# Performance work log

Hardware: AMD Instinct MI355X
Metric: run time of the kernel (lower is better)

Reference implementation:

```python
import jax, jax.numpy as jnp
import numpy as np

B, N, D, H = 4, 2048, 256, 4
HD = D // H


def _linear(x, W, b):
    return x @ W.T + b


def _rotate_half(x):
    # pairs (x0,x1) -> (-x1, x0)
    x1 = x[..., ::2]
    x2 = x[..., 1::2]
    return jnp.stack((-x2, x1), axis=-1).reshape(x.shape)


def _layernorm(x, g, b, eps=1e-5):
    m = jnp.mean(x, axis=-1, keepdims=True)
    v = jnp.mean((x - m) ** 2, axis=-1, keepdims=True)
    return (x - m) / jnp.sqrt(v + eps) * g + b


def _ffn(x, W1, b1, g, be, W2, b2):
    h = _linear(x, W1, b1)
    h = _layernorm(h, g, be)
    h = jax.nn.gelu(h, approximate=False)
    return _linear(h, W2, b2)


def _self_block(x, enc, Wqkv, bqkv, Wout, bout, W1, b1, g, be, W2, b2):
    Bq, Nq, _ = x.shape
    qkv = _linear(x, Wqkv, bqkv).reshape(Bq, Nq, H, HD, 3).transpose(0, 2, 1, 3, 4)  # [B,H,N,HD,3]
    q, k, v = qkv[..., 0], qkv[..., 1], qkv[..., 2]
    q = q * enc[0] + _rotate_half(q) * enc[1]
    k = k * enc[0] + _rotate_half(k) * enc[1]
    scale = HD ** -0.5
    sim = jnp.einsum('bhid,bhjd->bhij', q, k) * scale
    attn = jax.nn.softmax(sim, axis=-1)
    ctx = jnp.einsum('bhij,bhjd->bhid', attn, v)
    msg = _linear(ctx.transpose(0, 2, 1, 3).reshape(Bq, Nq, D), Wout, bout)
    return x + _ffn(jnp.concatenate([x, msg], axis=-1), W1, b1, g, be, W2, b2)


def _cross_block(x0, x1, Wqk, bqk, Wv, bv, Wo, bo, W1, b1, g, be, W2, b2):
    def heads(t):
        return t.reshape(t.shape[0], t.shape[1], H, HD).transpose(0, 2, 1, 3)  # [B,H,N,HD]
    qk0 = heads(_linear(x0, Wqk, bqk))
    qk1 = heads(_linear(x1, Wqk, bqk))
    v0 = heads(_linear(x0, Wv, bv))
    v1 = heads(_linear(x1, Wv, bv))
    s = (HD ** -0.5) ** 0.5
    qk0 = qk0 * s
    qk1 = qk1 * s
    sim = jnp.einsum('bhid,bhjd->bhij', qk0, qk1)
    attn01 = jax.nn.softmax(sim, axis=-1)   # over j (x1 tokens)
    attn10 = jax.nn.softmax(sim, axis=-2)   # over i (x0 tokens)
    m0 = jnp.einsum('bhij,bhjd->bhid', attn01, v1)
    m1 = jnp.einsum('bhij,bhid->bhjd', attn10, v0)
    def unheads(t):
        return t.transpose(0, 2, 1, 3).reshape(t.shape[0], t.shape[2], D)
    m0 = _linear(unheads(m0), Wo, bo)
    m1 = _linear(unheads(m1), Wo, bo)
    x0 = x0 + _ffn(jnp.concatenate([x0, m0], axis=-1), W1, b1, g, be, W2, b2)
    x1 = x1 + _ffn(jnp.concatenate([x1, m1], axis=-1), W1, b1, g, be, W2, b2)
    return x0, x1


def setup_inputs() -> dict:
    key = jax.random.key(0)
    ks = jax.random.split(key, 32)
    std = 0.05

    def rn(k, shape, s=std):
        return jax.random.normal(k, shape, dtype=jnp.float32) * s

    def enc(k):
        ang = jax.random.uniform(k, (B, 1, N, HD // 2), dtype=jnp.float32) * (2 * np.pi)
        cos = jnp.repeat(jnp.cos(ang), 2, axis=-1)
        sin = jnp.repeat(jnp.sin(ang), 2, axis=-1)
        return jnp.stack([cos, sin], axis=0)  # [2,B,1,N,HD]

    return {
        'desc0': rn(ks[0], (B, N, D), 1.0),
        'desc1': rn(ks[1], (B, N, D), 1.0),
        'enc0': enc(ks[2]),
        'enc1': enc(ks[3]),
        's_Wqkv': rn(ks[4], (3 * D, D)), 's_bqkv': jnp.zeros((3 * D,), jnp.float32),
        's_Wout': rn(ks[5], (D, D)), 's_bout': jnp.zeros((D,), jnp.float32),
        's_W1': rn(ks[6], (2 * D, 2 * D)), 's_b1': jnp.zeros((2 * D,), jnp.float32),
        's_g': jnp.ones((2 * D,), jnp.float32), 's_be': jnp.zeros((2 * D,), jnp.float32),
        's_W2': rn(ks[7], (D, 2 * D)), 's_b2': jnp.zeros((D,), jnp.float32),
        'c_Wqk': rn(ks[8], (D, D)), 'c_bqk': jnp.zeros((D,), jnp.float32),
        'c_Wv': rn(ks[9], (D, D)), 'c_bv': jnp.zeros((D,), jnp.float32),
        'c_Wo': rn(ks[10], (D, D)), 'c_bo': jnp.zeros((D,), jnp.float32),
        'c_W1': rn(ks[11], (2 * D, 2 * D)), 'c_b1': jnp.zeros((2 * D,), jnp.float32),
        'c_g': jnp.ones((2 * D,), jnp.float32), 'c_be': jnp.zeros((2 * D,), jnp.float32),
        'c_W2': rn(ks[12], (D, 2 * D)), 'c_b2': jnp.zeros((D,), jnp.float32),
    }


def reference(desc0, desc1, enc0, enc1,
              s_Wqkv, s_bqkv, s_Wout, s_bout, s_W1, s_b1, s_g, s_be, s_W2, s_b2,
              c_Wqk, c_bqk, c_Wv, c_bv, c_Wo, c_bo, c_W1, c_b1, c_g, c_be, c_W2, c_b2):
    d0 = _self_block(desc0, enc0, s_Wqkv, s_bqkv, s_Wout, s_bout, s_W1, s_b1, s_g, s_be, s_W2, s_b2)
    d1 = _self_block(desc1, enc1, s_Wqkv, s_bqkv, s_Wout, s_bout, s_W1, s_b1, s_g, s_be, s_W2, s_b2)
    return _cross_block(d0, d1, c_Wqk, c_bqk, c_Wv, c_bv, c_Wo, c_bo, c_W1, c_b1, c_g, c_be, c_W2, c_b2)
```

## Files before the change

kernel.cpp:

```cpp
#include <hip/hip_runtime.h>
#include <cstddef>

#define NTOK 2048
#define BDIM 4
#define DIM 256
#define NHEAD 4
#define MROWS 8192
#define M2 16384
#define NMu ((size_t)MROWS * DIM)

typedef unsigned short u16;
typedef __attribute__((ext_vector_type(8))) short short8;
typedef __attribute__((ext_vector_type(4))) float f32x4;

#if __has_builtin(__builtin_amdgcn_exp2f)
#define EXP2(x) __builtin_amdgcn_exp2f(x)
#else
#define EXP2(x) exp2f(x)
#endif

__device__ __forceinline__ u16 f2bf(float x) {
  union { float f; unsigned u; } c; c.f = x;
  unsigned r = c.u + 0x7FFFu + ((c.u >> 16) & 1u);
  return (u16)(r >> 16);
}
__device__ __forceinline__ float bf2f(u16 u) {
  union { unsigned u; float f; } c; c.u = ((unsigned)u) << 16;
  return c.f;
}

__device__ __forceinline__ void glds16(const void* g, void* l) {
  __builtin_amdgcn_global_load_lds(
      (const __attribute__((address_space(1))) unsigned int*)g,
      (__attribute__((address_space(3))) unsigned int*)l, 16, 0, 0);
}

__global__ __launch_bounds__(256) void gemm_bf16_kernel(
    const u16* __restrict__ A, int lda,
    const u16* __restrict__ A2, int lda2, int kSplit,
    const u16* __restrict__ W,
    const float* __restrict__ bias0, const float* __restrict__ bias1,
    int nsplit, float os0, float os1,
    u16* __restrict__ Yb0, int ldy0,
    u16* __restrict__ Yb1, int ldy1,
    int K)
{
  __shared__ u16 As[2 * 4096];
  __shared__ u16 Bs[2 * 4096];
  const int t = threadIdx.x;
  const int m0 = blockIdx.y * 128, n0 = blockIdx.x * 128;
  const int r4 = t >> 2, c8 = (t & 3) * 8;
  const int lane = t & 63, w = t >> 6;
  const int cl = lane & 15, quad = lane >> 4;
  const int wm = (w >> 1) * 64, wn = (w & 1) * 64;

  f32x4 acc[4][4];
#pragma unroll
  for (int i = 0; i < 4; ++i)
#pragma unroll
    for (int j = 0; j < 4; ++j) acc[i][j] = (f32x4){0.f, 0.f, 0.f, 0.f};

  for (int k0 = 0; k0 < K; k0 += 64) {
    const u16* Ab; int la; int kk;
    if (k0 < kSplit) { Ab = A; la = lda; kk = k0; }
    else             { Ab = A2; la = lda2; kk = k0 - kSplit; }
    const u16* ag = Ab + (size_t)(m0 + r4) * la + kk + c8;
    const u16* bg = W + (size_t)(n0 + r4) * K + k0 + c8;
    __syncthreads();
#pragma unroll
    for (int kh = 0; kh < 2; ++kh) {
      glds16(ag + kh * 32, &As[kh * 4096 + t * 8]);
      glds16(ag + (size_t)64 * la + kh * 32, &As[kh * 4096 + 2048 + t * 8]);
      glds16(bg + kh * 32, &Bs[kh * 4096 + t * 8]);
      glds16(bg + (size_t)64 * K + kh * 32, &Bs[kh * 4096 + 2048 + t * 8]);
    }
    __syncthreads();

#pragma unroll
    for (int kh = 0; kh < 2; ++kh) {
      short8 af[4], bfr[4];
#pragma unroll
      for (int i = 0; i < 4; ++i)
        af[i] = *(const short8*)&As[kh * 4096 + (wm + i * 16 + cl) * 32 + quad * 8];
#pragma unroll
      for (int i = 0; i < 4; ++i)
        bfr[i] = *(const short8*)&Bs[kh * 4096 + (wn + i * 16 + cl) * 32 + quad * 8];
#pragma unroll
      for (int mt = 0; mt < 4; ++mt)
#pragma unroll
        for (int nt = 0; nt < 4; ++nt)
          acc[mt][nt] = __builtin_amdgcn_mfma_f32_16x16x32_bf16(
              af[mt], bfr[nt], acc[mt][nt], 0, 0, 0);
    }
  }

#pragma unroll
  for (int mt = 0; mt < 4; ++mt)
#pragma unroll
    for (int nt = 0; nt < 4; ++nt) {
      const int colg = n0 + wn + nt * 16 + cl;
      const bool first = colg < nsplit;
      const int c2 = first ? colg : colg - nsplit;
      const float bs = first ? bias0[c2] : bias1[c2];
      const float os = first ? os0 : os1;
      u16* yb = first ? Yb0 : Yb1;
      const int ly = first ? ldy0 : ldy1;
#pragma unroll
      for (int r = 0; r < 4; ++r) {
        const int rowg = m0 + wm + mt * 16 + quad * 4 + r;
        yb[(size_t)rowg * ly + c2] = f2bf((acc[mt][nt][r] + bs) * os);
      }
    }
}

__global__ __launch_bounds__(256) void gemm64_kernel(
    const u16* __restrict__ A, int lda,
    const u16* __restrict__ W,
    const float* __restrict__ bias,
    const u16* __restrict__ resb, int ldrb,
    float* __restrict__ Yf, int ldyf,
    u16* __restrict__ Yb, int ldyb,
    int K)
{
  __shared__ u16 As[2 * 2048];
  __shared__ u16 Bs[2 * 2048];
  const int t = threadIdx.x;
  const int m0 = blockIdx.y * 64, n0 = blockIdx.x * 64;
  const int r8 = t >> 2, c8 = (t & 3) * 8;
  const int lane = t & 63, w = t >> 6;
  const int cl = lane & 15, quad = lane >> 4;
  const int wm = (w >> 1) * 32, wn = (w & 1) * 32;

  f32x4 acc[2][2];
#pragma unroll
  for (int i = 0; i < 2; ++i)
#pragma unroll
    for (int j = 0; j < 2; ++j) acc[i][j] = (f32x4){0.f, 0.f, 0.f, 0.f};

  for (int k0 = 0; k0 < K; k0 += 64) {
    const u16* ag = A + (size_t)(m0 + r8) * lda + k0 + c8;
    const u16* bg = W + (size_t)(n0 + r8) * K + k0 + c8;
    __syncthreads();
#pragma unroll
    for (int kh = 0; kh < 2; ++kh) {
      glds16(ag + kh * 32, &As[kh * 2048 + t * 8]);
      glds16(bg + kh * 32, &Bs[kh * 2048 + t * 8]);
    }
    __syncthreads();

#pragma unroll
    for (int kh = 0; kh < 2; ++kh) {
      short8 af[2], bfr[2];
#pragma unroll
      for (int i = 0; i < 2; ++i)
        af[i] = *(const short8*)&As[kh * 2048 + (wm + i * 16 + cl) * 32 + quad * 8];
#pragma unroll
      for (int j = 0; j < 2; ++j)
        bfr[j] = *(const short8*)&Bs[kh * 2048 + (wn + j * 16 + cl) * 32 + quad * 8];
#pragma unroll
      for (int mt = 0; mt < 2; ++mt)
#pragma unroll
        for (int nt = 0; nt < 2; ++nt)
          acc[mt][nt] = __builtin_amdgcn_mfma_f32_16x16x32_bf16(
              af[mt], bfr[nt], acc[mt][nt], 0, 0, 0);
    }
  }

#pragma unroll
  for (int mt = 0; mt < 2; ++mt)
#pragma unroll
    for (int nt = 0; nt < 2; ++nt) {
      const int colg = n0 + wn + nt * 16 + cl;
      const float bs = bias[colg];
#pragma unroll
      for (int r = 0; r < 4; ++r) {
        const int rowg = m0 + wm + mt * 16 + quad * 4 + r;
        float v = acc[mt][nt][r] + bs;
        if (resb) v += bf2f(resb[(size_t)rowg * ldrb + colg]);
        if (Yf) Yf[(size_t)rowg * ldyf + colg] = v;
        if (Yb) Yb[(size_t)rowg * ldyb + colg] = f2bf(v);
      }
    }
}

__global__ __launch_bounds__(256) void wfuse_kernel(
    const float* __restrict__ W1, const float* __restrict__ Wo,
    const float* __restrict__ b1, const float* __restrict__ bo,
    const float* __restrict__ cW1, const float* __restrict__ cWo,
    const float* __restrict__ cb1, const float* __restrict__ cbo,
    u16* __restrict__ W1f, u16* __restrict__ cW1f,
    float* __restrict__ b1f, float* __restrict__ cb1f)
{
  const int n = blockIdx.x, sel = blockIdx.y;
  const float* Ws = sel ? cW1 : W1;
  const float* Wos = sel ? cWo : Wo;
  u16* out = sel ? cW1f : W1f;
  __shared__ float rowh[256];
  const int t = threadIdx.x;
  rowh[t] = Ws[(size_t)n * 512 + 256 + t];
  out[(size_t)n * 512 + t] = f2bf(Ws[(size_t)n * 512 + t]);
  __syncthreads();
  float acc = 0.f;
  for (int m = 0; m < 256; ++m) acc += rowh[m] * Wos[(size_t)m * 256 + t];
  out[(size_t)n * 512 + 256 + t] = f2bf(acc);
  if (t == 0) {
    const float* bos = sel ? cbo : bo;
    const float* b1s = sel ? cb1 : b1;
    float a = b1s[n];
    for (int m = 0; m < 256; ++m) a += rowh[m] * bos[m];
    (sel ? cb1f : b1f)[n] = a;
  }
}

__global__ __launch_bounds__(256) void rope_repack_kernel(
    const u16* __restrict__ qkv, const float* __restrict__ enc0,
    const float* __restrict__ enc1,
    u16* __restrict__ Q, u16* __restrict__ K, u16* __restrict__ V)
{
  const int idx = blockIdx.x * blockDim.x + threadIdx.x;
  const int i = idx & 31;
  const int h = (idx >> 5) & 3;
  const int m = idx >> 7;
  const int half = m >> 13;
  const int lm = m & (MROWS - 1);
  const float* enc = half ? enc1 : enc0;
  const u16* src = qkv + (size_t)m * 768 + h * 192 + i * 6;
  const unsigned a0 = *(const unsigned*)(src);
  const unsigned a1 = *(const unsigned*)(src + 2);
  const unsigned a2 = *(const unsigned*)(src + 4);
  const float q0 = bf2f((u16)a0), k0 = bf2f((u16)(a0 >> 16));
  const float v0 = bf2f((u16)a1), q1 = bf2f((u16)(a1 >> 16));
  const float k1 = bf2f((u16)a2), v1 = bf2f((u16)(a2 >> 16));
  const float c = enc[(size_t)lm * 64 + 2 * i];
  const float s = enc[(size_t)MROWS * 64 + (size_t)lm * 64 + 2 * i];
  const float QSC = 0.18033688011112042f;
  const size_t o = (size_t)m * 256 + h * 64 + 2 * i;
  *(unsigned*)(Q + o) = (unsigned)f2bf((q0 * c - q1 * s) * QSC) |
                        ((unsigned)f2bf((q1 * c + q0 * s) * QSC) << 16);
  *(unsigned*)(K + o) = (unsigned)f2bf(k0 * c - k1 * s) |
                        ((unsigned)f2bf(k1 * c + k0 * s) << 16);
  *(unsigned*)(V + o) = (unsigned)f2bf(v0) | ((unsigned)f2bf(v1) << 16);
}

__global__ __launch_bounds__(256) void transpose_v_kernel(
    const u16* __restrict__ in, u16* __restrict__ out)
{
  __shared__ u16 Tl[64][72];
  const int bz = blockIdx.z, h = blockIdx.y;
  const int n0 = blockIdx.x * 64;
  const int t = threadIdx.x;
  {
    const int row = t >> 2, c16 = (t & 3) * 16;
    const u16* src = in + (size_t)(bz * NTOK + n0 + row) * 256 + h * 64 + c16;
    *(uint4*)&Tl[row][c16] = *(const uint4*)src;
    *(uint4*)&Tl[row][c16 + 8] = *(const uint4*)(src + 8);
  }
  __syncthreads();
  const int d = t >> 2, qr = t & 3;
  union { u16 u[16]; uint4 v[2]; } pk;
#pragma unroll
  for (int j = 0; j < 16; ++j) pk.u[j] = Tl[qr * 16 + j][d];
  u16* dst = out + ((size_t)((bz * NHEAD + h) * 64 + d)) * NTOK + n0 + qr * 16;
  *(uint4*)dst = pk.v[0];
  *(uint4*)(dst + 8) = pk.v[1];
}

__global__ __launch_bounds__(256, 2) void attn5_kernel(
    const u16* __restrict__ Qb, const u16* __restrict__ Kb,
    const u16* __restrict__ Vtb, u16* __restrict__ Ou, int cross)
{
  __shared__ u16 Ks[2][64 * 64];
  __shared__ u16 Vs[2][64 * 64];
  __shared__ u16 Ps[4][32 * 64];

  const int hw = blockIdx.x;
  const int li = hw >> 3;
  const int y  = (hw & 7) * 4 + (li >> 4);
  const int n0 = (li & 15) * 128;

  const int h2 = y >> 4, b = (y >> 2) & 3, h = y & 3;
  const int kh = cross ? (1 - h2) : h2;
  const int qrowbase = (h2 * 4 + b) * NTOK;
  const int krowbase = (kh * 4 + b) * NTOK;
  const int vz = kh * 4 + b;
  const int t = threadIdx.x, lane = t & 63, w = t >> 6;
  const int cl = lane & 15, quad = lane >> 4;
  const int q0 = w * 32;
  const int fsw = (cl & 7) << 4;

  short8 bq[2][2];
#pragma unroll
  for (int c = 0; c < 2; ++c) {
    const u16* qsrc = Qb + (size_t)(qrowbase + n0 + q0 + c * 16 + cl) * 256 +
                      h * 64 + quad * 8;
    bq[c][0] = *(const short8*)qsrc;
    bq[c][1] = *(const short8*)(qsrc + 32);
  }

  float l_r[2] = {0.f, 0.f};
  f32x4 o[2][4];
#pragma unroll
  for (int c = 0; c < 2; ++c)
#pragma unroll
    for (int i = 0; i < 4; ++i) o[c][i] = (f32x4){0.f, 0.f, 0.f, 0.f};

  const int srow = t >> 2;
  const int scb = (t & 3) * 32;
  const int ssw = (srow & 7) << 4;
  const u16* Kg = Kb + (size_t)(krowbase + srow) * 256 + h * 64 + (t & 3) * 16;
  const u16* Vg = Vtb + ((size_t)(vz * NHEAD + h) * 64 + srow) * NTOK + (t & 3) * 16;

  uint4 ka0 = *(const uint4*)Kg, ka1 = *(const uint4*)(Kg + 8);
  uint4 va0 = *(const uint4*)Vg, va1 = *(const uint4*)(Vg + 8);
  {
    char* kd = (char*)&Ks[0][srow * 64];
    *(uint4*)(kd + (scb ^ ssw)) = ka0;
    *(uint4*)(kd + ((scb + 16) ^ ssw)) = ka1;
    char* vd = (char*)&Vs[0][srow * 64];
    *(uint4*)(vd + (scb ^ ssw)) = va0;
    *(uint4*)(vd + ((scb + 16) ^ ssw)) = va1;
  }
  Kg += 64 * 256; Vg += 64;
  ka0 = *(const uint4*)Kg; ka1 = *(const uint4*)(Kg + 8);
  va0 = *(const uint4*)Vg; va1 = *(const uint4*)(Vg + 8);
  __syncthreads();

  for (int tile = 0; tile < 32; ++tile) {
    const int cur = tile & 1, nxt = cur ^ 1;

    f32x4 sf[2][4];
    __builtin_amdgcn_s_setprio(1);
#pragma unroll
    for (int kb = 0; kb < 4; ++kb) {
      const char* kr = (const char*)&Ks[cur][(kb * 16 + cl) * 64];
      short8 ak0 = *(const short8*)(kr + ((quad * 16) ^ fsw));
      short8 ak1 = *(const short8*)(kr + ((quad * 16 + 64) ^ fsw));
#pragma unroll
      for (int c = 0; c < 2; ++c) {
        f32x4 acc = (f32x4){0.f, 0.f, 0.f, 0.f};
        acc = __builtin_amdgcn_mfma_f32_16x16x32_bf16(ak0, bq[c][0], acc, 0, 0, 0);
        acc = __builtin_amdgcn_mfma_f32_16x16x32_bf16(ak1, bq[c][1], acc, 0, 0, 0);
        sf[c][kb] = acc;
      }
    }
    __builtin_amdgcn_s_setprio(0);

    if (tile < 31) {
      char* kd = (char*)&Ks[nxt][srow * 64];
      *(uint4*)(kd + (scb ^ ssw)) = ka0;
      *(uint4*)(kd + ((scb + 16) ^ ssw)) = ka1;
      if (tile < 30) {
        Kg += 64 * 256;
        ka0 = *(const uint4*)Kg; ka1 = *(const uint4*)(Kg + 8);
      }
    }

#pragma unroll
    for (int c = 0; c < 2; ++c) {
      float rs = 0.f;
#pragma unroll
      for (int kb = 0; kb < 4; ++kb)
#pragma unroll
        for (int r = 0; r < 4; ++r) {
          const float p = EXP2(sf[c][kb][r]);
          sf[c][kb][r] = p; rs += p;
        }
      rs += __shfl_xor(rs, 16);
      rs += __shfl_xor(rs, 32);
      l_r[c] += rs;
      char* pd = (char*)&Ps[w][(c * 16 + cl) * 64];
#pragma unroll
      for (int kb = 0; kb < 4; ++kb) {
        unsigned d0 = __builtin_amdgcn_perm(__float_as_uint(sf[c][kb][1]),
                                            __float_as_uint(sf[c][kb][0]), 0x07060302u);
        unsigned d1 = __builtin_amdgcn_perm(__float_as_uint(sf[c][kb][3]),
                                            __float_as_uint(sf[c][kb][2]), 0x07060302u);
        uint2 pk; pk.x = d0; pk.y = d1;
        *(uint2*)(pd + ((kb * 32 + quad * 8) ^ fsw)) = pk;
      }
    }

    short8 bp[2][2];
#pragma unroll
    for (int c = 0; c < 2; ++c) {
      const char* pr = (const char*)&Ps[w][(c * 16 + cl) * 64];
      bp[c][0] = *(const short8*)(pr + ((quad * 16) ^ fsw));
      bp[c][1] = *(const short8*)(pr + ((quad * 16 + 64) ^ fsw));
    }
    __builtin_amdgcn_s_setprio(1);
#pragma unroll
    for (int db = 0; db < 4; ++db) {
      const char* vr = (const char*)&Vs[cur][(db * 16 + cl) * 64];
      short8 av0 = *(const short8*)(vr + ((quad * 16) ^ fsw));
      short8 av1 = *(const short8*)(vr + ((quad * 16 + 64) ^ fsw));
#pragma unroll
      for (int c = 0; c < 2; ++c) {
        o[c][db] = __builtin_amdgcn_mfma_f32_16x16x32_bf16(av0, bp[c][0], o[c][db], 0, 0, 0);
        o[c][db] = __builtin_amdgcn_mfma_f32_16x16x32_bf16(av1, bp[c][1], o[c][db], 0, 0, 0);
      }
    }
    __builtin_amdgcn_s_setprio(0);

    if (tile < 31) {
      char* vd = (char*)&Vs[nxt][srow * 64];
      *(uint4*)(vd + (scb ^ ssw)) = va0;
      *(uint4*)(vd + ((scb + 16) ^ ssw)) = va1;
      if (tile < 30) {
        Vg += 64;
        va0 = *(const uint4*)Vg; va1 = *(const uint4*)(Vg + 8);
      }
    }
    __syncthreads();
  }

#pragma unroll
  for (int c = 0; c < 2; ++c) {
    const float inv = 1.f / l_r[c];
    const size_t rowo = (size_t)(qrowbase + n0 + q0 + c * 16 + cl) * 256 + h * 64;
#pragma unroll
    for (int db = 0; db < 4; ++db) {
      ushort4 st;
      st.x = f2bf(o[c][db][0] * inv); st.y = f2bf(o[c][db][1] * inv);
      st.z = f2bf(o[c][db][2] * inv); st.w = f2bf(o[c][db][3] * inv);
      *(ushort4*)(Ou + rowo + db * 16 + quad * 4) = st;
    }
  }
}

__global__ __launch_bounds__(256) void ln_gelu_kernel(
    const u16* __restrict__ Hm, const float* __restrict__ g,
    const float* __restrict__ be, u16* __restrict__ out)
{
  const int rowi = blockIdx.x * 4 + (threadIdx.x >> 6);
  const int lane = threadIdx.x & 63;
  const u16* row = Hm + (size_t)rowi * 512 + lane * 8;
  u16* orow = out + (size_t)rowi * 512 + lane * 8;
  uint4 raw = *(const uint4*)row;
  float x[8];
  const unsigned* rw = (const unsigned*)&raw;
#pragma unroll
  for (int i = 0; i < 4; ++i) {
    x[2 * i]     = bf2f((u16)rw[i]);
    x[2 * i + 1] = bf2f((u16)(rw[i] >> 16));
  }
  float s = 0.f;
#pragma unroll
  for (int i = 0; i < 8; ++i) s += x[i];
#pragma unroll
  for (int off = 32; off; off >>= 1) s += __shfl_xor(s, off);
  const float mean = s * (1.f / 512.f);
  float s2 = 0.f;
#pragma unroll
  for (int i = 0; i < 8; ++i) { const float d = x[i] - mean; s2 += d * d; }
#pragma unroll
  for (int off = 32; off; off >>= 1) s2 += __shfl_xor(s2, off);
  const float rstd = rsqrtf(s2 * (1.f / 512.f) + 1e-5f);
  unsigned ov[4];
#pragma unroll
  for (int i = 0; i < 4; ++i) {
    const int c = lane * 8 + 2 * i;
    const float y0 = (x[2 * i] - mean) * rstd * g[c] + be[c];
    const float y1 = (x[2 * i + 1] - mean) * rstd * g[c + 1] + be[c + 1];
    const float g0 = 0.5f * y0 * (1.f + erff(y0 * 0.70710678118654752f));
    const float g1 = 0.5f * y1 * (1.f + erff(y1 * 0.70710678118654752f));
    ov[i] = (unsigned)f2bf(g0) | ((unsigned)f2bf(g1) << 16);
  }
  *(uint4*)orow = *(uint4*)ov;
}

__global__ __launch_bounds__(256) void pack_all_kernel(
    const float* w0, const float* w1, const float* w2, const float* w3,
    const float* w4, const float* d0, const float* d1,
    u16* __restrict__ wb, u16* __restrict__ descb)
{
  const size_t idx4 = ((size_t)blockIdx.x * 256 + threadIdx.x) * 4;
  const float* src; u16* dst; size_t off;
  if (idx4 < 589824) {
    off = idx4; dst = wb + idx4;
    if      (idx4 < 196608) { src = w0; }
    else if (idx4 < 327680) { src = w1; off -= 196608; }
    else if (idx4 < 393216) { src = w2; off -= 327680; }
    else if (idx4 < 458752) { src = w3; off -= 393216; }
    else                    { src = w4; off -= 458752; }
  } else {
    size_t o = idx4 - 589824;
    dst = descb + o;
    if (o < NMu) { src = d0; off = o; }
    else         { src = d1; off = o - NMu; }
  }
  float4 v = *(const float4*)(src + off);
  ushort4 ov;
  ov.x = f2bf(v.x); ov.y = f2bf(v.y); ov.z = f2bf(v.z); ov.w = f2bf(v.w);
  *(ushort4*)dst = ov;
}

extern "C" void kernel_launch(void* const* d_in, const int* in_sizes, int n_in,
                              void* d_out, int out_size, void* d_ws, size_t ws_size,
                              hipStream_t stream) {
  const float* desc0  = (const float*)d_in[0];
  const float* desc1  = (const float*)d_in[1];
  const float* enc0   = (const float*)d_in[2];
  const float* enc1   = (const float*)d_in[3];
  const float* s_Wqkv = (const float*)d_in[4];
  const float* s_bqkv = (const float*)d_in[5];
  const float* s_Wout = (const float*)d_in[6];
  const float* s_bout = (const float*)d_in[7];
  const float* s_W1   = (const float*)d_in[8];
  const float* s_b1   = (const float*)d_in[9];
  const float* s_g    = (const float*)d_in[10];
  const float* s_be   = (const float*)d_in[11];
  const float* s_W2   = (const float*)d_in[12];
  const float* s_b2   = (const float*)d_in[13];
  const float* c_Wqk  = (const float*)d_in[14];
  const float* c_bqk  = (const float*)d_in[15];
  const float* c_Wv   = (const float*)d_in[16];
  const float* c_bv   = (const float*)d_in[17];
  const float* c_Wo   = (const float*)d_in[18];
  const float* c_bo   = (const float*)d_in[19];
  const float* c_W1   = (const float*)d_in[20];
  const float* c_b1   = (const float*)d_in[21];
  const float* c_g    = (const float*)d_in[22];
  const float* c_be   = (const float*)d_in[23];
  const float* c_W2   = (const float*)d_in[24];
  const float* c_b2   = (const float*)d_in[25];

  u16* U = (u16*)d_ws;
  u16* descb = U + 0 * NMu;
  u16* qkvb  = U + 2 * NMu;
  u16* ctxb  = U + 2 * NMu;
  u16* Qu    = U + 8 * NMu;
  u16* Ku    = U + 10 * NMu;
  u16* Vu    = U + 12 * NMu;
  u16* Vt    = U + 14 * NMu;
  u16* hbufb = U + 12 * NMu;
  u16* hb2   = U + 16 * NMu;
  float* b1f = (float*)(U + 20 * NMu);
  float* cb1f = b1f + 512;
  u16* s_b   = U + 21 * NMu;
  u16* wb    = U + 23 * NMu;

  u16* Wqkvb = wb;
  u16* W2b   = wb + 196608;
  u16* cQKVb = wb + 327680;
  u16* cW2b  = wb + 458752;
  u16* W1f   = wb + 589824;
  u16* cW1f  = wb + 851968;

  float* outf = (float*)d_out;

  const dim3 tv_grid(NTOK / 64, NHEAD, 8);
  const int rope_blocks = (M2 * 128) / 256;
  const int lng_blocks  = M2 / 4;
  const float csc = 0.42466090014400953f;

  hipLaunchKernelGGL(pack_all_kernel, dim3(4672), dim3(256), 0, stream,
                     s_Wqkv, s_W2, c_Wqk, c_Wv, c_W2, desc0, desc1, wb, descb);
  hipLaunchKernelGGL(wfuse_kernel, dim3(512, 2), dim3(256), 0, stream,
                     s_W1, s_Wout, s_b1, s_bout, c_W1, c_Wo, c_b1, c_bo,
                     W1f, cW1f, b1f, cb1f);

  hipLaunchKernelGGL(gemm_bf16_kernel, dim3(6, 128), dim3(256), 0, stream,
                     descb, 256, (const u16*)nullptr, 0, 1 << 30, Wqkvb,
                     s_bqkv, (const float*)nullptr, 1 << 30, 1.f, 1.f,
                     qkvb, 768, (u16*)nullptr, 0, 256);
  hipLaunchKernelGGL(rope_repack_kernel, dim3(rope_blocks), dim3(256), 0, stream,
                     qkvb, enc0, enc1, Qu, Ku, Vu);
  hipLaunchKernelGGL(transpose_v_kernel, tv_grid, dim3(256), 0, stream, Vu, Vt);
  hipLaunchKernelGGL(attn5_kernel, dim3(512), dim3(256), 0, stream,
                     Qu, Ku, Vt, ctxb, 0);
  hipLaunchKernelGGL(gemm_bf16_kernel, dim3(4, 128), dim3(256), 0, stream,
                     descb, 256, ctxb, 256, 256, W1f,
                     b1f, (const float*)nullptr, 1 << 30, 1.f, 1.f,
                     hbufb, 512, (u16*)nullptr, 0, 512);
  hipLaunchKernelGGL(ln_gelu_kernel, dim3(lng_blocks), dim3(256), 0, stream,
                     hbufb, s_g, s_be, hb2);
  hipLaunchKernelGGL(gemm64_kernel, dim3(4, 256), dim3(256), 0, stream,
                     hb2, 512, W2b, s_b2, descb, 256,
                     (float*)nullptr, 0, s_b, 256, 512);

  u16* qkb = Qu;
  u16* vb  = Ku;
  hipLaunchKernelGGL(gemm_bf16_kernel, dim3(4, 128), dim3(256), 0, stream,
                     s_b, 256, (const u16*)nullptr, 0, 1 << 30, cQKVb,
                     c_bqk, c_bv, 256, csc, 1.f,
                     qkb, 256, vb, 256, 256);
  hipLaunchKernelGGL(transpose_v_kernel, tv_grid, dim3(256), 0, stream, vb, Vt);
  hipLaunchKernelGGL(attn5_kernel, dim3(512), dim3(256), 0, stream,
                     qkb, qkb, Vt, ctxb, 1);
  hipLaunchKernelGGL(gemm_bf16_kernel, dim3(4, 128), dim3(256), 0, stream,
                     s_b, 256, ctxb, 256, 256, cW1f,
                     cb1f, (const float*)nullptr, 1 << 30, 1.f, 1.f,
                     hbufb, 512, (u16*)nullptr, 0, 512);
  hipLaunchKernelGGL(ln_gelu_kernel, dim3(lng_blocks), dim3(256), 0, stream,
                     hbufb, c_g, c_be, hb2);
  hipLaunchKernelGGL(gemm64_kernel, dim3(4, 256), dim3(256), 0, stream,
                     hb2, 512, cW2b, c_b2, s_b, 256,
                     outf, 256, (u16*)nullptr, 0, 512);
}
```

Baseline: 372.9 us.

## Merge weight pack with weight fusion, and fuse RoPE repack with V transpose

Folds the bf16 packing kernel and the weight-fusion kernel into one launch by splitting on block index. Also fuses the RoPE/QKV repack with the V transpose: V tiles are staged in shared memory and written straight out transposed, so the intermediate V buffer and its extra global round trip go away. The fused RoPE kernel launches only 256 blocks, each looping 32 times, which lowers parallelism compared with the previous 8192-block launch. Two kernel launches are removed.

```diff
diff --git a/kernel.cpp b/kernel.cpp
--- a/kernel.cpp
+++ b/kernel.cpp
@@ -183,7 +183,10 @@
     }
 }
 
-__global__ __launch_bounds__(256) void wfuse_kernel(
+__global__ __launch_bounds__(256) void pack_wfuse_kernel(
+    const float* w0, const float* w1, const float* w2, const float* w3,
+    const float* w4, const float* d0, const float* d1,
+    u16* __restrict__ wb, u16* __restrict__ descb,
     const float* __restrict__ W1, const float* __restrict__ Wo,
     const float* __restrict__ b1, const float* __restrict__ bo,
     const float* __restrict__ cW1, const float* __restrict__ cWo,
@@ -191,55 +194,101 @@
     u16* __restrict__ W1f, u16* __restrict__ cW1f,
     float* __restrict__ b1f, float* __restrict__ cb1f)
 {
-  const int n = blockIdx.x, sel = blockIdx.y;
-  const float* Ws = sel ? cW1 : W1;
-  const float* Wos = sel ? cWo : Wo;
-  u16* out = sel ? cW1f : W1f;
   __shared__ float rowh[256];
+  const int bid = blockIdx.x;
   const int t = threadIdx.x;
-  rowh[t] = Ws[(size_t)n * 512 + 256 + t];
-  out[(size_t)n * 512 + t] = f2bf(Ws[(size_t)n * 512 + t]);
-  __syncthreads();
-  float acc = 0.f;
-  for (int m = 0; m < 256; ++m) acc += rowh[m] * Wos[(size_t)m * 256 + t];
-  out[(size_t)n * 512 + 256 + t] = f2bf(acc);
-  if (t == 0) {
-    const float* bos = sel ? cbo : bo;
-    const float* b1s = sel ? cb1 : b1;
-    float a = b1s[n];
-    for (int m = 0; m < 256; ++m) a += rowh[m] * bos[m];
-    (sel ? cb1f : b1f)[n] = a;
-  }
-}
-
-__global__ __launch_bounds__(256) void rope_repack_kernel(
+  if (bid < 4672) {
+    const size_t idx4 = ((size_t)bid * 256 + t) * 4;
+    const float* src; u16* dst; size_t off;
+    if (idx4 < 589824) {
+      off = idx4; dst = wb + idx4;
+      if      (idx4 < 196608) { src = w0; }
+      else if (idx4 < 327680) { src = w1; off -= 196608; }
+      else if (idx4 < 393216) { src = w2; off -= 327680; }
+      else if (idx4 < 458752) { src = w3; off -= 393216; }
+      else                    { src = w4; off -= 458752; }
+    } else {
+      size_t o = idx4 - 589824;
+      dst = descb + o;
+      if (o < NMu) { src = d0; off = o; }
+      else         { src = d1; off = o - NMu; }
+    }
+    float4 v = *(const float4*)(src + off);
+    ushort4 ov;
+    ov.x = f2bf(v.x); ov.y = f2bf(v.y); ov.z = f2bf(v.z); ov.w = f2bf(v.w);
+    *(ushort4*)dst = ov;
+  } else {
+    const int idx = bid - 4672;
+    const int n = idx & 511, sel = idx >> 9;
+    const float* Ws = sel ? cW1 : W1;
+    const float* Wos = sel ? cWo : Wo;
+    u16* out = sel ? cW1f : W1f;
+    rowh[t] = Ws[(size_t)n * 512 + 256 + t];
+    out[(size_t)n * 512 + t] = f2bf(Ws[(size_t)n * 512 + t]);
+    __syncthreads();
+    float acc = 0.f;
+    for (int m = 0; m < 256; ++m) acc += rowh[m] * Wos[(size_t)m * 256 + t];
+    out[(size_t)n * 512 + 256 + t] = f2bf(acc);
+    if (t == 0) {
+      const float* bos = sel ? cbo : bo;
+      const float* b1s = sel ? cb1 : b1;
+      float a = b1s[n];
+      for (int m = 0; m < 256; ++m) a += rowh[m] * bos[m];
+      (sel ? cb1f : b1f)[n] = a;
+    }
+  }
+}
+
+__global__ __launch_bounds__(256) void rope_tv_kernel(
     const u16* __restrict__ qkv, const float* __restrict__ enc0,
     const float* __restrict__ enc1,
-    u16* __restrict__ Q, u16* __restrict__ K, u16* __restrict__ V)
+    u16* __restrict__ Q, u16* __restrict__ K, u16* __restrict__ Vt)
 {
-  const int idx = blockIdx.x * blockDim.x + threadIdx.x;
-  const int i = idx & 31;
-  const int h = (idx >> 5) & 3;
-  const int m = idx >> 7;
-  const int half = m >> 13;
-  const int lm = m & (MROWS - 1);
-  const float* enc = half ? enc1 : enc0;
-  const u16* src = qkv + (size_t)m * 768 + h * 192 + i * 6;
-  const unsigned a0 = *(const unsigned*)(src);
-  const unsigned a1 = *(const unsigned*)(src + 2);
-  const unsigned a2 = *(const unsigned*)(src + 4);
-  const float q0 = bf2f((u16)a0), k0 = bf2f((u16)(a0 >> 16));
-  const float v0 = bf2f((u16)a1), q1 = bf2f((u16)(a1 >> 16));
-  const float k1 = bf2f((u16)a2), v1 = bf2f((u16)(a2 >> 16));
-  const float c = enc[(size_t)lm * 64 + 2 * i];
-  const float s = enc[(size_t)MROWS * 64 + (size_t)lm * 64 + 2 * i];
+  __shared__ u16 Vl[64 * 264];
+  const int blk = blockIdx.x;
+  const int t = threadIdx.x;
+  const int hf = blk >> 7;
+  const float* enc = hf ? enc1 : enc0;
   const float QSC = 0.18033688011112042f;
-  const size_t o = (size_t)m * 256 + h * 64 + 2 * i;
-  *(unsigned*)(Q + o) = (unsigned)f2bf((q0 * c - q1 * s) * QSC) |
-                        ((unsigned)f2bf((q1 * c + q0 * s) * QSC) << 16);
-  *(unsigned*)(K + o) = (unsigned)f2bf(k0 * c - k1 * s) |
-                        ((unsigned)f2bf(k1 * c + k0 * s) << 16);
-  *(unsigned*)(V + o) = (unsigned)f2bf(v0) | ((unsigned)f2bf(v1) << 16);
+
+  for (int p = 0; p < 32; ++p) {
+    const int j = p * 256 + t;
+    const int i = j & 31;
+    const int h = (j >> 5) & 3;
+    const int lt = j >> 7;
+    const int m = blk * 64 + lt;
+    const int lm = m & (MROWS - 1);
+    const u16* src = qkv + (size_t)m * 768 + h * 192 + i * 6;
+    const unsigned a0 = *(const unsigned*)(src);
+    const unsigned a1 = *(const unsigned*)(src + 2);
+    const unsigned a2 = *(const unsigned*)(src + 4);
+    const float q0 = bf2f((u16)a0), k0 = bf2f((u16)(a0 >> 16));
+    const float v0 = bf2f((u16)a1), q1 = bf2f((u16)(a1 >> 16));
+    const float k1 = bf2f((u16)a2), v1 = bf2f((u16)(a2 >> 16));
+    const float c = enc[(size_t)lm * 64 + 2 * i];
+    const float s = enc[(size_t)MROWS * 64 + (size_t)lm * 64 + 2 * i];
+    const size_t o = (size_t)m * 256 + h * 64 + 2 * i;
+    *(unsigned*)(Q + o) = (unsigned)f2bf((q0 * c - q1 * s) * QSC) |
+                          ((unsigned)f2bf((q1 * c + q0 * s) * QSC) << 16);
+    *(unsigned*)(K + o) = (unsigned)f2bf(k0 * c - k1 * s) |
+                          ((unsigned)f2bf(k1 * c + k0 * s) << 16);
+    *(unsigned*)&Vl[lt * 264 + h * 64 + 2 * i] =
+        (unsigned)f2bf(v0) | ((unsigned)f2bf(v1) << 16);
+  }
+  __syncthreads();
+
+  const int bz = blk >> 5, n0 = (blk & 31) * 64;
+  const int dd = t >> 2, qr = t & 3;
+#pragma unroll
+  for (int h = 0; h < 4; ++h) {
+    union { u16 u[16]; uint4 v[2]; } pk;
+#pragma unroll
+    for (int jj = 0; jj < 16; ++jj)
+      pk.u[jj] = Vl[(qr * 16 + jj) * 264 + h * 64 + dd];
+    u16* dst = Vt + ((size_t)((bz * NHEAD + h) * 64 + dd)) * NTOK + n0 + qr * 16;
+    *(uint4*)dst = pk.v[0];
+    *(uint4*)(dst + 8) = pk.v[1];
+  }
 }
 
 __global__ __launch_bounds__(256) void transpose_v_kernel(
@@ -466,32 +515,6 @@
     ov[i] = (unsigned)f2bf(g0) | ((unsigned)f2bf(g1) << 16);
   }
   *(uint4*)orow = *(uint4*)ov;
-}
-
-__global__ __launch_bounds__(256) void pack_all_kernel(
-    const float* w0, const float* w1, const float* w2, const float* w3,
-    const float* w4, const float* d0, const float* d1,
-    u16* __restrict__ wb, u16* __restrict__ descb)
-{
-  const size_t idx4 = ((size_t)blockIdx.x * 256 + threadIdx.x) * 4;
-  const float* src; u16* dst; size_t off;
-  if (idx4 < 589824) {
-    off = idx4; dst = wb + idx4;
-    if      (idx4 < 196608) { src = w0; }
-    else if (idx4 < 327680) { src = w1; off -= 196608; }
-    else if (idx4 < 393216) { src = w2; off -= 327680; }
-    else if (idx4 < 458752) { src = w3; off -= 393216; }
-    else                    { src = w4; off -= 458752; }
-  } else {
-    size_t o = idx4 - 589824;
-    dst = descb + o;
-    if (o < NMu) { src = d0; off = o; }
-    else         { src = d1; off = o - NMu; }
-  }
-  float4 v = *(const float4*)(src + off);
-  ushort4 ov;
-  ov.x = f2bf(v.x); ov.y = f2bf(v.y); ov.z = f2bf(v.z); ov.w = f2bf(v.w);
-  *(ushort4*)dst = ov;
 }
 
 extern "C" void kernel_launch(void* const* d_in, const int* in_sizes, int n_in,
@@ -530,7 +553,6 @@
   u16* ctxb  = U + 2 * NMu;
   u16* Qu    = U + 8 * NMu;
   u16* Ku    = U + 10 * NMu;
-  u16* Vu    = U + 12 * NMu;
   u16* Vt    = U + 14 * NMu;
   u16* hbufb = U + 12 * NMu;
   u16* hb2   = U + 16 * NMu;
@@ -549,13 +571,11 @@
   float* outf = (float*)d_out;
 
   const dim3 tv_grid(NTOK / 64, NHEAD, 8);
-  const int rope_blocks = (M2 * 128) / 256;
   const int lng_blocks  = M2 / 4;
   const float csc = 0.42466090014400953f;
 
-  hipLaunchKernelGGL(pack_all_kernel, dim3(4672), dim3(256), 0, stream,
-                     s_Wqkv, s_W2, c_Wqk, c_Wv, c_W2, desc0, desc1, wb, descb);
-  hipLaunchKernelGGL(wfuse_kernel, dim3(512, 2), dim3(256), 0, stream,
+  hipLaunchKernelGGL(pack_wfuse_kernel, dim3(5696), dim3(256), 0, stream,
+                     s_Wqkv, s_W2, c_Wqk, c_Wv, c_W2, desc0, desc1, wb, descb,
                      s_W1, s_Wout, s_b1, s_bout, c_W1, c_Wo, c_b1, c_bo,
                      W1f, cW1f, b1f, cb1f);
 
@@ -563,9 +583,8 @@
                      descb, 256, (const u16*)nullptr, 0, 1 << 30, Wqkvb,
                      s_bqkv, (const float*)nullptr, 1 << 30, 1.f, 1.f,
                      qkvb, 768, (u16*)nullptr, 0, 256);
-  hipLaunchKernelGGL(rope_repack_kernel, dim3(rope_blocks), dim3(256), 0, stream,
-                     qkvb, enc0, enc1, Qu, Ku, Vu);
-  hipLaunchKernelGGL(transpose_v_kernel, tv_grid, dim3(256), 0, stream, Vu, Vt);
+  hipLaunchKernelGGL(rope_tv_kernel, dim3(256), dim3(256), 0, stream,
+                     qkvb, enc0, enc1, Qu, Ku, Vt);
   hipLaunchKernelGGL(attn5_kernel, dim3(512), dim3(256), 0, stream,
                      Qu, Ku, Vt, ctxb, 0);
   hipLaunchKernelGGL(gemm_bf16_kernel, dim3(4, 128), dim3(256), 0, stream,
```

New measurement: 377.2 us. Within noise of the previous version (+1.2%).
